# Kernel tuning notes

Hardware: AMD Instinct MI355X
Metric: run time of the kernel (lower is better)

## Reference

```python
import jax, jax.numpy as jnp
import numpy as np

EPS = 1e-6
CHUNK = 128  # chunk size for the chunked causal recurrence


def elu_feature_map(x):
    # fast_transformers default feature map: elu(x) + 1
    return jax.nn.elu(x) + 1.0


def causal_dot_product(Q, K, V):
    """out[l] = Q[l] @ sum_{l' <= l} K[l']^T V[l'].
    Q, K: (N, L, H, E); V: (N, L, H, D) -> (N, L, H, D).
    Chunked parallel recurrence: intra-chunk masked attention + inter-chunk state.
    """
    N, L, H, E = Q.shape
    D = V.shape[-1]
    C = CHUNK
    nc = L // C

    def to_chunks(x):
        # (N, L, H, F) -> (nc, N, H, C, F)
        F = x.shape[-1]
        return x.reshape(N, nc, C, H, F).transpose(1, 0, 3, 2, 4)

    Qc, Kc, Vc = to_chunks(Q), to_chunks(K), to_chunks(V)
    tri = jnp.tril(jnp.ones((C, C), dtype=Q.dtype))  # causal mask within chunk

    def step(state, qkv):  # state: (N, H, E, D)
        q, k, v = qkv  # (N,H,C,E), (N,H,C,E), (N,H,C,D)
        inter = jnp.einsum('nhce,nhed->nhcd', q, state)
        scores = jnp.einsum('nhce,nhfe->nhcf', q, k) * tri
        intra = jnp.einsum('nhcf,nhfd->nhcd', scores, v)
        state = state + jnp.einsum('nhce,nhcd->nhed', k, v)
        return state, inter + intra

    state0 = jnp.zeros((N, H, E, D), dtype=Q.dtype)
    _, out = jax.lax.scan(step, state0, (Qc, Kc, Vc))
    # (nc, N, H, C, D) -> (N, L, H, D)
    return out.transpose(1, 0, 3, 2, 4).reshape(N, L, H, D)


def setup_inputs() -> dict:
    key = jax.random.key(0)
    k1, k2, k3 = jax.random.split(key, 3)
    N, L, H, E = 4, 8192, 16, 64
    return {
        'queries': jax.random.normal(k1, (N, L, H, E), jnp.float32),
        'keys': jax.random.normal(k2, (N, L, H, E), jnp.float32),
        'values': jax.random.normal(k3, (N, L, H, E), jnp.float32),
        'key_mask': jnp.ones((N, L), dtype=bool),
    }


def reference(queries, keys, values, key_mask):
    # key_mask is accepted but unused, matching the original forward().
    Q = elu_feature_map(queries)
    K = elu_feature_map(keys)
    Z = 1.0 / (jnp.einsum('nlhi,nlhi->nlh', Q, jnp.cumsum(K, axis=1)) + EPS)
    V = causal_dot_product(Q, K, values)
    return V * Z[..., None]
```

## Files before the change

### kernel.cpp

```cpp
#include <hip/hip_runtime.h>
#include <hip/hip_bf16.h>


#define Nn   4
#define Ll   8192
#define Hh   16
#define NHh  64
#define CCH  64
#define LDB  72
#define SLOT 4160
#define EPSF 1e-6f

typedef __attribute__((ext_vector_type(8))) short short8;
typedef __attribute__((ext_vector_type(4))) float floatx4;

__device__ __forceinline__ float elu1(float x) {
  return x > 0.f ? x + 1.f : __expf(x);
}

__device__ __forceinline__ float4 elu4(float4 v) {
  v.x = elu1(v.x); v.y = elu1(v.y); v.z = elu1(v.z); v.w = elu1(v.w);
  return v;
}

__device__ __forceinline__ floatx4 mfma16(short8 a, short8 b, floatx4 c) {
  return __builtin_amdgcn_mfma_f32_16x16x32_bf16(a, b, c, 0, 0, 0);
}

__device__ __forceinline__ void bar_lgkm() {
  __builtin_amdgcn_s_waitcnt(0xc07f);
  __builtin_amdgcn_s_barrier();
  __builtin_amdgcn_sched_barrier(0);
}

__device__ __forceinline__ short8 frag_ld(const __hip_bfloat16* base, int row,
                                          int kh, int quad) {
  return *(const short8*)(base + row * LDB + kh * 32 + quad * 8);
}

__device__ __forceinline__ void st4bf(__hip_bfloat16* dst, float a, float b,
                                      float c, float d) {
  union { __hip_bfloat16 h[4]; uint2 u; } pk;
  pk.h[0] = __float2bfloat16(a); pk.h[1] = __float2bfloat16(b);
  pk.h[2] = __float2bfloat16(c); pk.h[3] = __float2bfloat16(d);
  *(uint2*)dst = pk.u;
}

__device__ __forceinline__ float bf2f(short s) {
  union { unsigned u; float f; } cv;
  cv.u = ((unsigned)(unsigned short)s) << 16;
  return cv.f;
}

__device__ __forceinline__ float sum8bf(short8 v) {
  float s = 0.f;
#pragma unroll
  for (int i = 0; i < 8; ++i) s += bf2f(v[i]);
  return s;
}

__global__ __launch_bounds__(256, 4) void la_pass1(
    const float* __restrict__ Kg, const float* __restrict__ Vg,
    float* __restrict__ ws, int G, int Lseg) {
  const int bid = blockIdx.x;
  const int nh = bid / G, g = bid % G;
  const int n = nh / Hh, h = nh % Hh;
  const int t = threadIdx.x;
  const int wave = t >> 6, lane = t & 63, m = lane & 15, quad = lane >> 4;
  const int jr0 = m * 4;
  const int er0 = wave * 16 + quad * 4;

  __shared__ __hip_bfloat16 Kt[2][64 * LDB];
  __shared__ __hip_bfloat16 Vt[2][64 * LDB];

  floatx4 Sacc[4];
  const floatx4 z4 = {0.f, 0.f, 0.f, 0.f};
#pragma unroll
  for (int b = 0; b < 4; ++b) Sacc[b] = z4;
  float kpriv[4] = {0.f, 0.f, 0.f, 0.f};

  const int nchunk = Lseg / CCH;

#define P1_LOAD(KR, VR, c_) do { \
    const size_t gb_ = \
        ((size_t)((n * Ll + g * Lseg + (c_) * CCH + jr0) * Hh + h)) * 64 + er0; \
    KR[0] = *(const float4*)(Kg + gb_);        \
    KR[1] = *(const float4*)(Kg + gb_ + 1024); \
    KR[2] = *(const float4*)(Kg + gb_ + 2048); \
    KR[3] = *(const float4*)(Kg + gb_ + 3072); \
    VR[0] = *(const float4*)(Vg + gb_);        \
    VR[1] = *(const float4*)(Vg + gb_ + 1024); \
    VR[2] = *(const float4*)(Vg + gb_ + 2048); \
    VR[3] = *(const float4*)(Vg + gb_ + 3072); \
  } while (0)

#define P1_STAGE(KR, VR, p_) do { \
    float4 e0 = elu4(KR[0]), e1 = elu4(KR[1]), e2 = elu4(KR[2]), e3 = elu4(KR[3]); \
    kpriv[0] += e0.x + e1.x + e2.x + e3.x; \
    kpriv[1] += e0.y + e1.y + e2.y + e3.y; \
    kpriv[2] += e0.z + e1.z + e2.z + e3.z; \
    kpriv[3] += e0.w + e1.w + e2.w + e3.w; \
    __hip_bfloat16* kt_ = Kt[p_]; __hip_bfloat16* vt_ = Vt[p_]; \
    st4bf(&kt_[(er0 + 0) * LDB + jr0], e0.x, e1.x, e2.x, e3.x); \
    st4bf(&kt_[(er0 + 1) * LDB + jr0], e0.y, e1.y, e2.y, e3.y); \
    st4bf(&kt_[(er0 + 2) * LDB + jr0], e0.z, e1.z, e2.z, e3.z); \
    st4bf(&kt_[(er0 + 3) * LDB + jr0], e0.w, e1.w, e2.w, e3.w); \
    st4bf(&vt_[(er0 + 0) * LDB + jr0], VR[0].x, VR[1].x, VR[2].x, VR[3].x); \
    st4bf(&vt_[(er0 + 1) * LDB + jr0], VR[0].y, VR[1].y, VR[2].y, VR[3].y); \
    st4bf(&vt_[(er0 + 2) * LDB + jr0], VR[0].z, VR[1].z, VR[2].z, VR[3].z); \
    st4bf(&vt_[(er0 + 3) * LDB + jr0], VR[0].w, VR[1].w, VR[2].w, VR[3].w); \
  } while (0)

#define P1_MFMA(p_) do { \
    const short8 a0 = frag_ld(Vt[p_], 16 * wave + m, 0, quad); \
    const short8 a1 = frag_ld(Vt[p_], 16 * wave + m, 1, quad); \
    __builtin_amdgcn_s_setprio(1); \
    _Pragma("unroll") \
    for (int b = 0; b < 4; ++b) { \
      Sacc[b] = mfma16(a0, frag_ld(Kt[p_], 16 * b + m, 0, quad), Sacc[b]); \
      Sacc[b] = mfma16(a1, frag_ld(Kt[p_], 16 * b + m, 1, quad), Sacc[b]); \
    } \
    __builtin_amdgcn_s_setprio(0); \
  } while (0)

  float4 ka[4], va[4], kb[4], vb[4];
  P1_LOAD(ka, va, 0);
  P1_LOAD(kb, vb, 1);
  P1_STAGE(ka, va, 0);
  for (int c = 0; c < nchunk; c += 2) {
    if (c + 2 < nchunk) P1_LOAD(ka, va, c + 2);
    bar_lgkm();
    P1_MFMA(0);
    P1_STAGE(kb, vb, 1);
    if (c + 3 < nchunk) P1_LOAD(kb, vb, c + 3);
    bar_lgkm();
    P1_MFMA(1);
    if (c + 2 < nchunk) P1_STAGE(ka, va, 0);
  }
#undef P1_LOAD
#undef P1_STAGE
#undef P1_MFMA

#pragma unroll
  for (int i = 0; i < 4; ++i) {
    kpriv[i] += __shfl_xor(kpriv[i], 1);
    kpriv[i] += __shfl_xor(kpriv[i], 2);
    kpriv[i] += __shfl_xor(kpriv[i], 4);
    kpriv[i] += __shfl_xor(kpriv[i], 8);
  }
  const size_t slot = (size_t)bid * SLOT;
#pragma unroll
  for (int b = 0; b < 4; ++b)
#pragma unroll
    for (int r = 0; r < 4; ++r) {
      const int d = 16 * wave + quad * 4 + r, e = 16 * b + m;
      ws[slot + d * 64 + e] = Sacc[b][r];
    }
  if (m == 0)
#pragma unroll
    for (int i = 0; i < 4; ++i) ws[slot + 4096 + er0 + i] = kpriv[i];
}

__global__ __launch_bounds__(256) void la_pass2(float* __restrict__ ws, int G) {
  const int nh = blockIdx.x / 17, part = blockIdx.x % 17;
  const int idx = part * 256 + threadIdx.x;
  if (idx >= SLOT) return;
  float run = 0.f;
  for (int g = 0; g < G; ++g) {
    const size_t base = (size_t)(nh * G + g) * SLOT;
    const float cur = ws[base + idx];
    ws[base + idx] = run;
    run += cur;
  }
}

__global__ __launch_bounds__(256, 4) void la_pass3(
    const float* __restrict__ Qg, const float* __restrict__ Kg,
    const float* __restrict__ Vg, const float* __restrict__ ws,
    float* __restrict__ out, int G, int Lseg, int has_prefix) {
  const int bid = blockIdx.x;
  const int nh = bid / G, g = bid % G;
  const int n = nh / Hh, h = nh % Hh;
  const int t = threadIdx.x;
  const int wave = t >> 6, lane = t & 63, m = lane & 15, quad = lane >> 4;
  const int row = t >> 2, q4 = t & 3;
  const int jr0 = m * 4;
  const int er0 = wave * 16 + quad * 4;

  __shared__ __hip_bfloat16 QPb[64 * LDB];
  __shared__ __hip_bfloat16 Kb [64 * LDB];
  __shared__ __hip_bfloat16 Ktb[64 * LDB];
  __shared__ __hip_bfloat16 Vtb[64 * LDB];
  __shared__ float ksum[64];
  __shared__ float kpart[4][64];

  const size_t slot = (size_t)bid * SLOT;
  floatx4 Sacc[4];
  const floatx4 z4 = {0.f, 0.f, 0.f, 0.f};
#pragma unroll
  for (int b = 0; b < 4; ++b) {
    Sacc[b] = z4;
    if (has_prefix) {
#pragma unroll
      for (int r = 0; r < 4; ++r)
        Sacc[b][r] = ws[slot + (16 * wave + quad * 4 + r) * 64 + 16 * b + m];
    }
  }
  if (t < 64) ksum[t] = has_prefix ? ws[slot + 4096 + t] : 0.f;

  const int nchunk = Lseg / CCH;
  for (int c = 0; c < nchunk; ++c) {
    const int lbase = g * Lseg + c * CCH;
    const size_t gbr = ((size_t)((n * Ll + lbase + row) * Hh + h)) * 64;
    const size_t gbv = ((size_t)((n * Ll + lbase + jr0) * Hh + h)) * 64 + er0;
    float4 qr[4], kr[4];
#pragma unroll
    for (int u = 0; u < 4; ++u) {
      const int col = u * 16 + q4 * 4;
      qr[u] = *(const float4*)(Qg + gbr + col);
      kr[u] = *(const float4*)(Kg + gbr + col);
    }
    float4 vr0 = *(const float4*)(Vg + gbv);
    float4 vr1 = *(const float4*)(Vg + gbv + 1024);
    float4 vr2 = *(const float4*)(Vg + gbv + 2048);
    float4 vr3 = *(const float4*)(Vg + gbv + 3072);
#pragma unroll
    for (int u = 0; u < 4; ++u) {
      const int col = u * 16 + q4 * 4;
      float4 qv = elu4(qr[u]);
      float4 kv = elu4(kr[u]);
      st4bf(&QPb[row * LDB + col], qv.x, qv.y, qv.z, qv.w);
      st4bf(&Kb [row * LDB + col], kv.x, kv.y, kv.z, kv.w);
      Ktb[(col + 0) * LDB + row] = __float2bfloat16(kv.x);
      Ktb[(col + 1) * LDB + row] = __float2bfloat16(kv.y);
      Ktb[(col + 2) * LDB + row] = __float2bfloat16(kv.z);
      Ktb[(col + 3) * LDB + row] = __float2bfloat16(kv.w);
    }
    bar_lgkm();

    const short8 qa0 = frag_ld(QPb, 16 * wave + m, 0, quad);
    const short8 qa1 = frag_ld(QPb, 16 * wave + m, 1, quad);
    floatx4 sc[4];
    __builtin_amdgcn_s_setprio(1);
#pragma unroll
    for (int b = 0; b < 4; ++b) {
      sc[b] = mfma16(qa0, frag_ld(Kb, 16 * b + m, 0, quad), z4);
      sc[b] = mfma16(qa1, frag_ld(Kb, 16 * b + m, 1, quad), sc[b]);
    }
    __builtin_amdgcn_s_setprio(0);
    float dpart = 0.f;
    {
      const float* ks0 = &ksum[quad * 8];
      const float* ks1 = &ksum[32 + quad * 8];
#pragma unroll
      for (int u = 0; u < 8; ++u) dpart += bf2f(qa0[u]) * ks0[u];
#pragma unroll
      for (int u = 0; u < 8; ++u) dpart += bf2f(qa1[u]) * ks1[u];
    }
    dpart += __shfl_xor(dpart, 16);
    dpart += __shfl_xor(dpart, 32);
    float z[4];
#pragma unroll
    for (int r = 0; r < 4; ++r) {
      const int i = 16 * wave + quad * 4 + r;
      float rs = 0.f;
#pragma unroll
      for (int b = 0; b < 4; ++b) {
        const int j = 16 * b + m;
        rs += (j <= i) ? sc[b][r] : 0.f;
      }
      rs += __shfl_xor(rs, 1);
      rs += __shfl_xor(rs, 2);
      rs += __shfl_xor(rs, 4);
      rs += __shfl_xor(rs, 8);
      const float den = __shfl(dpart, quad * 4 + r);
      z[r] = 1.f / (den + rs + EPSF);
    }
    bar_lgkm();

#pragma unroll
    for (int b = 0; b < 4; ++b)
#pragma unroll
      for (int r = 0; r < 4; ++r) {
        const int i = 16 * wave + quad * 4 + r, j = 16 * b + m;
        QPb[i * LDB + j] = __float2bfloat16(j <= i ? sc[b][r] : 0.f);
        Kb[i * LDB + j] = __float2bfloat16(Sacc[b][r]);
      }
    st4bf(&Vtb[(er0 + 0) * LDB + jr0], vr0.x, vr1.x, vr2.x, vr3.x);
    st4bf(&Vtb[(er0 + 1) * LDB + jr0], vr0.y, vr1.y, vr2.y, vr3.y);
    st4bf(&Vtb[(er0 + 2) * LDB + jr0], vr0.z, vr1.z, vr2.z, vr3.z);
    st4bf(&Vtb[(er0 + 3) * LDB + jr0], vr0.w, vr1.w, vr2.w, vr3.w);
    bar_lgkm();

    const short8 pa0 = frag_ld(QPb, 16 * wave + m, 0, quad);
    const short8 pa1 = frag_ld(QPb, 16 * wave + m, 1, quad);
    const short8 va0 = frag_ld(Vtb, 16 * wave + m, 0, quad);
    const short8 va1 = frag_ld(Vtb, 16 * wave + m, 1, quad);
    floatx4 O[4];
    __builtin_amdgcn_s_setprio(1);
#pragma unroll
    for (int b = 0; b < 4; ++b) {
      O[b] = mfma16(qa0, frag_ld(Kb, 16 * b + m, 0, quad), z4);
      O[b] = mfma16(qa1, frag_ld(Kb, 16 * b + m, 1, quad), O[b]);
      O[b] = mfma16(pa0, frag_ld(Vtb, 16 * b + m, 0, quad), O[b]);
      O[b] = mfma16(pa1, frag_ld(Vtb, 16 * b + m, 1, quad), O[b]);
      Sacc[b] = mfma16(va0, frag_ld(Ktb, 16 * b + m, 0, quad), Sacc[b]);
      Sacc[b] = mfma16(va1, frag_ld(Ktb, 16 * b + m, 1, quad), Sacc[b]);
    }
    __builtin_amdgcn_s_setprio(0);
    {
      const short8 x0 = *(const short8*)(&Ktb[lane * LDB + wave * 16]);
      const short8 x1 = *(const short8*)(&Ktb[lane * LDB + wave * 16 + 8]);
      kpart[wave][lane] = sum8bf(x0) + sum8bf(x1);
    }
    const size_t ob = ((size_t)((n * Ll + lbase) * Hh + h)) * 64;
#pragma unroll
    for (int r = 0; r < 4; ++r) {
      const int i = 16 * wave + quad * 4 + r;
#pragma unroll
      for (int b = 0; b < 4; ++b)
        out[ob + (size_t)i * (Hh * 64) + 16 * b + m] = O[b][r] * z[r];
    }
    bar_lgkm();
    if (t < 64)
      ksum[t] += kpart[0][t] + kpart[1][t] + kpart[2][t] + kpart[3][t];
  }
}

extern "C" void kernel_launch(void* const* d_in, const int* in_sizes, int n_in,
                              void* d_out, int out_size, void* d_ws, size_t ws_size,
                              hipStream_t stream) {
  (void)in_sizes; (void)n_in; (void)out_size;
  const float* Qg = (const float*)d_in[0];
  const float* Kg = (const float*)d_in[1];
  const float* Vg = (const float*)d_in[2];
  float* out = (float*)d_out;
  float* ws = (float*)d_ws;

  const size_t per_seg = (size_t)NHh * SLOT * sizeof(float);
  int G = 1;
  if (ws_size >= 16 * per_seg) G = 16;
  else if (ws_size >= 8 * per_seg) G = 8;
  else if (ws_size >= 4 * per_seg) G = 4;
  else if (ws_size >= 2 * per_seg) G = 2;
  const int Lseg = Ll / G;

  if (G > 1) {
    la_pass1<<<NHh * G, 256, 0, stream>>>(Kg, Vg, ws, G, Lseg);
    la_pass2<<<NHh * 17, 256, 0, stream>>>(ws, G);
  }
  la_pass3<<<NHh * G, 256, 0, stream>>>(Qg, Kg, Vg, ws, out, G, Lseg, G > 1 ? 1 : 0);
}
```

Measured before the change: 481.5 us.

## Fuse three passes into one kernel with atomic-flag cross-block prefix handoff

Merges the per-segment state pass, the prefix-scan pass and the output pass into a single kernel. Each block except the last computes its segment's KV state and key sum, publishes them with a release atomic bitmask, then waits on the masks of its predecessors and sums their states itself before running the output loop. This removes two kernel launches and the separate scan pass. In exchange, the last segment's work is serialized behind its predecessors, each block redundantly sums up to G-1 prefix slots, and correctness relies on every block in the grid being co-resident, otherwise the spin-wait can hang until its iteration cap.

```diff
diff --git a/kernel.cpp b/kernel.cpp
--- a/kernel.cpp
+++ b/kernel.cpp
@@ -59,29 +59,53 @@
   return s;
 }
 
-__global__ __launch_bounds__(256, 4) void la_pass1(
-    const float* __restrict__ Kg, const float* __restrict__ Vg,
-    float* __restrict__ ws, int G, int Lseg) {
+__device__ __forceinline__ float ld_agent_f32(const float* p) {
+  union { unsigned u; float f; } cv;
+  cv.u = __hip_atomic_load((const unsigned*)p, __ATOMIC_RELAXED,
+                           __HIP_MEMORY_SCOPE_AGENT);
+  return cv.f;
+}
+
+__global__ void la_zero(unsigned* __restrict__ masks) {
+  masks[threadIdx.x] = 0u;
+}
+
+__global__ __launch_bounds__(256, 4) void la_fused(
+    const float* __restrict__ Qg, const float* __restrict__ Kg,
+    const float* __restrict__ Vg, float* __restrict__ ws,
+    float* __restrict__ out, int G, int Lseg) {
   const int bid = blockIdx.x;
   const int nh = bid / G, g = bid % G;
   const int n = nh / Hh, h = nh % Hh;
   const int t = threadIdx.x;
   const int wave = t >> 6, lane = t & 63, m = lane & 15, quad = lane >> 4;
+  const int row = t >> 2, q4 = t & 3;
   const int jr0 = m * 4;
   const int er0 = wave * 16 + quad * 4;
 
-  __shared__ __hip_bfloat16 Kt[2][64 * LDB];
-  __shared__ __hip_bfloat16 Vt[2][64 * LDB];
+  __shared__ __hip_bfloat16 QPb[64 * LDB];
+  __shared__ __hip_bfloat16 Kb [64 * LDB];
+  __shared__ __hip_bfloat16 Ktb[64 * LDB];
+  __shared__ __hip_bfloat16 Vtb[64 * LDB];
+  __shared__ float ksum[64];
+  __shared__ float kpart[4][64];
+
+  unsigned* maskp =
+      (unsigned*)(ws + (size_t)NHh * G * SLOT) + nh;
 
   floatx4 Sacc[4];
   const floatx4 z4 = {0.f, 0.f, 0.f, 0.f};
 #pragma unroll
   for (int b = 0; b < 4; ++b) Sacc[b] = z4;
-  float kpriv[4] = {0.f, 0.f, 0.f, 0.f};
 
   const int nchunk = Lseg / CCH;
 
-#define P1_LOAD(KR, VR, c_) do { \
+  if (G > 1 && g < G - 1) {
+    __hip_bfloat16* kt0 = Ktb; __hip_bfloat16* vt0 = Vtb;
+    __hip_bfloat16* kt1 = QPb; __hip_bfloat16* vt1 = Kb;
+    float kpriv[4] = {0.f, 0.f, 0.f, 0.f};
+
+#define P_LOAD(KR, VR, c_) do { \
     const size_t gb_ = \
         ((size_t)((n * Ll + g * Lseg + (c_) * CCH + jr0) * Hh + h)) * 64 + er0; \
     KR[0] = *(const float4*)(Kg + gb_);        \
@@ -94,121 +118,107 @@
     VR[3] = *(const float4*)(Vg + gb_ + 3072); \
   } while (0)
 
-#define P1_STAGE(KR, VR, p_) do { \
+#define P_STAGE(KR, VR, kt_, vt_) do { \
     float4 e0 = elu4(KR[0]), e1 = elu4(KR[1]), e2 = elu4(KR[2]), e3 = elu4(KR[3]); \
     kpriv[0] += e0.x + e1.x + e2.x + e3.x; \
     kpriv[1] += e0.y + e1.y + e2.y + e3.y; \
     kpriv[2] += e0.z + e1.z + e2.z + e3.z; \
     kpriv[3] += e0.w + e1.w + e2.w + e3.w; \
-    __hip_bfloat16* kt_ = Kt[p_]; __hip_bfloat16* vt_ = Vt[p_]; \
-    st4bf(&kt_[(er0 + 0) * LDB + jr0], e0.x, e1.x, e2.x, e3.x); \
-    st4bf(&kt_[(er0 + 1) * LDB + jr0], e0.y, e1.y, e2.y, e3.y); \
-    st4bf(&kt_[(er0 + 2) * LDB + jr0], e0.z, e1.z, e2.z, e3.z); \
-    st4bf(&kt_[(er0 + 3) * LDB + jr0], e0.w, e1.w, e2.w, e3.w); \
-    st4bf(&vt_[(er0 + 0) * LDB + jr0], VR[0].x, VR[1].x, VR[2].x, VR[3].x); \
-    st4bf(&vt_[(er0 + 1) * LDB + jr0], VR[0].y, VR[1].y, VR[2].y, VR[3].y); \
-    st4bf(&vt_[(er0 + 2) * LDB + jr0], VR[0].z, VR[1].z, VR[2].z, VR[3].z); \
-    st4bf(&vt_[(er0 + 3) * LDB + jr0], VR[0].w, VR[1].w, VR[2].w, VR[3].w); \
+    st4bf(&(kt_)[(er0 + 0) * LDB + jr0], e0.x, e1.x, e2.x, e3.x); \
+    st4bf(&(kt_)[(er0 + 1) * LDB + jr0], e0.y, e1.y, e2.y, e3.y); \
+    st4bf(&(kt_)[(er0 + 2) * LDB + jr0], e0.z, e1.z, e2.z, e3.z); \
+    st4bf(&(kt_)[(er0 + 3) * LDB + jr0], e0.w, e1.w, e2.w, e3.w); \
+    st4bf(&(vt_)[(er0 + 0) * LDB + jr0], VR[0].x, VR[1].x, VR[2].x, VR[3].x); \
+    st4bf(&(vt_)[(er0 + 1) * LDB + jr0], VR[0].y, VR[1].y, VR[2].y, VR[3].y); \
+    st4bf(&(vt_)[(er0 + 2) * LDB + jr0], VR[0].z, VR[1].z, VR[2].z, VR[3].z); \
+    st4bf(&(vt_)[(er0 + 3) * LDB + jr0], VR[0].w, VR[1].w, VR[2].w, VR[3].w); \
   } while (0)
 
-#define P1_MFMA(p_) do { \
-    const short8 a0 = frag_ld(Vt[p_], 16 * wave + m, 0, quad); \
-    const short8 a1 = frag_ld(Vt[p_], 16 * wave + m, 1, quad); \
+#define P_MFMA(kt_, vt_) do { \
+    const short8 a0 = frag_ld((vt_), 16 * wave + m, 0, quad); \
+    const short8 a1 = frag_ld((vt_), 16 * wave + m, 1, quad); \
     __builtin_amdgcn_s_setprio(1); \
     _Pragma("unroll") \
     for (int b = 0; b < 4; ++b) { \
-      Sacc[b] = mfma16(a0, frag_ld(Kt[p_], 16 * b + m, 0, quad), Sacc[b]); \
-      Sacc[b] = mfma16(a1, frag_ld(Kt[p_], 16 * b + m, 1, quad), Sacc[b]); \
+      Sacc[b] = mfma16(a0, frag_ld((kt_), 16 * b + m, 0, quad), Sacc[b]); \
+      Sacc[b] = mfma16(a1, frag_ld((kt_), 16 * b + m, 1, quad), Sacc[b]); \
     } \
     __builtin_amdgcn_s_setprio(0); \
   } while (0)
 
-  float4 ka[4], va[4], kb[4], vb[4];
-  P1_LOAD(ka, va, 0);
-  P1_LOAD(kb, vb, 1);
-  P1_STAGE(ka, va, 0);
-  for (int c = 0; c < nchunk; c += 2) {
-    if (c + 2 < nchunk) P1_LOAD(ka, va, c + 2);
-    bar_lgkm();
-    P1_MFMA(0);
-    P1_STAGE(kb, vb, 1);
-    if (c + 3 < nchunk) P1_LOAD(kb, vb, c + 3);
-    bar_lgkm();
-    P1_MFMA(1);
-    if (c + 2 < nchunk) P1_STAGE(ka, va, 0);
+    float4 ka[4], va[4], kb2[4], vb2[4];
+    P_LOAD(ka, va, 0);
+    P_LOAD(kb2, vb2, 1);
+    P_STAGE(ka, va, kt0, vt0);
+    for (int c = 0; c < nchunk; c += 2) {
+      if (c + 2 < nchunk) P_LOAD(ka, va, c + 2);
+      bar_lgkm();
+      P_MFMA(kt0, vt0);
+      P_STAGE(kb2, vb2, kt1, vt1);
+      if (c + 3 < nchunk) P_LOAD(kb2, vb2, c + 3);
+      bar_lgkm();
+      P_MFMA(kt1, vt1);
+      if (c + 2 < nchunk) P_STAGE(ka, va, kt0, vt0);
+    }
+#undef P_LOAD
+#undef P_STAGE
+#undef P_MFMA
+
+#pragma unroll
+    for (int i = 0; i < 4; ++i) {
+      kpriv[i] += __shfl_xor(kpriv[i], 1);
+      kpriv[i] += __shfl_xor(kpriv[i], 2);
+      kpriv[i] += __shfl_xor(kpriv[i], 4);
+      kpriv[i] += __shfl_xor(kpriv[i], 8);
+    }
+    float* slotw = ws + (size_t)(nh * G + g) * SLOT;
+#pragma unroll
+    for (int b = 0; b < 4; ++b)
+#pragma unroll
+      for (int r = 0; r < 4; ++r) {
+        const int d = 16 * wave + quad * 4 + r, e = 16 * b + m;
+        slotw[d * 64 + e] = Sacc[b][r];
+      }
+    if (m == 0)
+#pragma unroll
+      for (int i = 0; i < 4; ++i) slotw[4096 + er0 + i] = kpriv[i];
+    __syncthreads();
+    if (t == 0)
+      __hip_atomic_fetch_or(maskp, 1u << g, __ATOMIC_RELEASE,
+                            __HIP_MEMORY_SCOPE_AGENT);
+#pragma unroll
+    for (int b = 0; b < 4; ++b) Sacc[b] = z4;
   }
-#undef P1_LOAD
-#undef P1_STAGE
-#undef P1_MFMA
-
-#pragma unroll
-  for (int i = 0; i < 4; ++i) {
-    kpriv[i] += __shfl_xor(kpriv[i], 1);
-    kpriv[i] += __shfl_xor(kpriv[i], 2);
-    kpriv[i] += __shfl_xor(kpriv[i], 4);
-    kpriv[i] += __shfl_xor(kpriv[i], 8);
+
+  float ks_init = 0.f;
+  if (G > 1 && g > 0) {
+    const unsigned need = (1u << g) - 1u;
+    if (t == 0) {
+      int iter = 0;
+      while ((__hip_atomic_load(maskp, __ATOMIC_ACQUIRE,
+                                __HIP_MEMORY_SCOPE_AGENT) & need) != need &&
+             iter < (1 << 24)) {
+        __builtin_amdgcn_s_sleep(2);
+        ++iter;
+      }
+    }
+    __syncthreads();
+    (void)__hip_atomic_load(maskp, __ATOMIC_ACQUIRE, __HIP_MEMORY_SCOPE_AGENT);
+    for (int gp = 0; gp < g; ++gp) {
+      const float* base = ws + (size_t)(nh * G + gp) * SLOT;
+#pragma unroll
+      for (int b = 0; b < 4; ++b)
+#pragma unroll
+        for (int r = 0; r < 4; ++r) {
+          const int d = 16 * wave + quad * 4 + r, e = 16 * b + m;
+          Sacc[b][r] += ld_agent_f32(base + d * 64 + e);
+        }
+      if (t < 64) ks_init += ld_agent_f32(base + 4096 + t);
+    }
   }
-  const size_t slot = (size_t)bid * SLOT;
-#pragma unroll
-  for (int b = 0; b < 4; ++b)
-#pragma unroll
-    for (int r = 0; r < 4; ++r) {
-      const int d = 16 * wave + quad * 4 + r, e = 16 * b + m;
-      ws[slot + d * 64 + e] = Sacc[b][r];
-    }
-  if (m == 0)
-#pragma unroll
-    for (int i = 0; i < 4; ++i) ws[slot + 4096 + er0 + i] = kpriv[i];
-}
-
-__global__ __launch_bounds__(256) void la_pass2(float* __restrict__ ws, int G) {
-  const int nh = blockIdx.x / 17, part = blockIdx.x % 17;
-  const int idx = part * 256 + threadIdx.x;
-  if (idx >= SLOT) return;
-  float run = 0.f;
-  for (int g = 0; g < G; ++g) {
-    const size_t base = (size_t)(nh * G + g) * SLOT;
-    const float cur = ws[base + idx];
-    ws[base + idx] = run;
-    run += cur;
-  }
-}
-
-__global__ __launch_bounds__(256, 4) void la_pass3(
-    const float* __restrict__ Qg, const float* __restrict__ Kg,
-    const float* __restrict__ Vg, const float* __restrict__ ws,
-    float* __restrict__ out, int G, int Lseg, int has_prefix) {
-  const int bid = blockIdx.x;
-  const int nh = bid / G, g = bid % G;
-  const int n = nh / Hh, h = nh % Hh;
-  const int t = threadIdx.x;
-  const int wave = t >> 6, lane = t & 63, m = lane & 15, quad = lane >> 4;
-  const int row = t >> 2, q4 = t & 3;
-  const int jr0 = m * 4;
-  const int er0 = wave * 16 + quad * 4;
-
-  __shared__ __hip_bfloat16 QPb[64 * LDB];
-  __shared__ __hip_bfloat16 Kb [64 * LDB];
-  __shared__ __hip_bfloat16 Ktb[64 * LDB];
-  __shared__ __hip_bfloat16 Vtb[64 * LDB];
-  __shared__ float ksum[64];
-  __shared__ float kpart[4][64];
-
-  const size_t slot = (size_t)bid * SLOT;
-  floatx4 Sacc[4];
-  const floatx4 z4 = {0.f, 0.f, 0.f, 0.f};
-#pragma unroll
-  for (int b = 0; b < 4; ++b) {
-    Sacc[b] = z4;
-    if (has_prefix) {
-#pragma unroll
-      for (int r = 0; r < 4; ++r)
-        Sacc[b][r] = ws[slot + (16 * wave + quad * 4 + r) * 64 + 16 * b + m];
-    }
-  }
-  if (t < 64) ksum[t] = has_prefix ? ws[slot + 4096 + t] : 0.f;
-
-  const int nchunk = Lseg / CCH;
+  if (t < 64) ksum[t] = ks_init;
+  __syncthreads();
+
   for (int c = 0; c < nchunk; ++c) {
     const int lbase = g * Lseg + c * CCH;
     const size_t gbr = ((size_t)((n * Ll + lbase + row) * Hh + h)) * 64;
@@ -339,15 +349,15 @@
 
   const size_t per_seg = (size_t)NHh * SLOT * sizeof(float);
   int G = 1;
-  if (ws_size >= 16 * per_seg) G = 16;
-  else if (ws_size >= 8 * per_seg) G = 8;
-  else if (ws_size >= 4 * per_seg) G = 4;
-  else if (ws_size >= 2 * per_seg) G = 2;
+  if (ws_size >= 16 * per_seg + 1024) G = 16;
+  else if (ws_size >= 8 * per_seg + 1024) G = 8;
+  else if (ws_size >= 4 * per_seg + 1024) G = 4;
+  else if (ws_size >= 2 * per_seg + 1024) G = 2;
   const int Lseg = Ll / G;
 
   if (G > 1) {
-    la_pass1<<<NHh * G, 256, 0, stream>>>(Kg, Vg, ws, G, Lseg);
-    la_pass2<<<NHh * 17, 256, 0, stream>>>(ws, G);
+    unsigned* masks = (unsigned*)(ws + (size_t)NHh * G * SLOT);
+    la_zero<<<1, NHh, 0, stream>>>(masks);
   }
-  la_pass3<<<NHh * G, 256, 0, stream>>>(Qg, Kg, Vg, ws, out, G, Lseg, G > 1 ? 1 : 0);
-}
+  la_fused<<<NHh * G, 256, 0, stream>>>(Qg, Kg, Vg, ws, out, G, Lseg);
+}
```

After: 609.2 us. +26.5%, slower.

## Split pass1 sequence across waves with private LDS tiles and cross-wave reduction

Applied to the files above, without the earlier changes.

Pass 1 now gives each wave its own contiguous quarter of the segment, processed in 32-position chunks in private LDS tiles. This removes the block-wide barriers inside the loop. Each wave holds the full 64x64 state in 16 MFMA accumulators and fills it from its own K/V loads. The per-wave partial states and key sums are then reduced through shared memory at the end. The cost is more accumulator registers, a K dimension of 32 per chunk, and no software prefetch double-buffering, which may expose global load latency.

```diff
diff --git a/kernel.cpp b/kernel.cpp
--- a/kernel.cpp
+++ b/kernel.cpp
@@ -38,6 +38,14 @@
   return *(const short8*)(base + row * LDB + kh * 32 + quad * 8);
 }
 
+__device__ __forceinline__ short8 frag36(const short* base, int row, int quad) {
+  union { short8 v; uint2 p[2]; } u;
+  const short* p = base + row * 36 + quad * 8;
+  u.p[0] = *(const uint2*)(p);
+  u.p[1] = *(const uint2*)(p + 4);
+  return u.v;
+}
+
 __device__ __forceinline__ void st4bf(__hip_bfloat16* dst, float a, float b,
                                       float c, float d) {
   union { __hip_bfloat16 h[4]; uint2 u; } pk;
@@ -67,98 +75,116 @@
   const int n = nh / Hh, h = nh % Hh;
   const int t = threadIdx.x;
   const int wave = t >> 6, lane = t & 63, m = lane & 15, quad = lane >> 4;
-  const int jr0 = m * 4;
-  const int er0 = wave * 16 + quad * 4;
-
-  __shared__ __hip_bfloat16 Kt[2][64 * LDB];
-  __shared__ __hip_bfloat16 Vt[2][64 * LDB];
-
-  floatx4 Sacc[4];
+  const int pg = lane & 7, cg = lane >> 3;
+  const int j0 = pg * 4, c0 = cg * 8;
+
+  __shared__ __align__(16) short smem[18432];
+  short* Kt = smem + wave * 2304;
+  short* Vt = smem + 9216 + wave * 2304;
+
+  floatx4 acc[4][4];
   const floatx4 z4 = {0.f, 0.f, 0.f, 0.f};
 #pragma unroll
-  for (int b = 0; b < 4; ++b) Sacc[b] = z4;
-  float kpriv[4] = {0.f, 0.f, 0.f, 0.f};
-
-  const int nchunk = Lseg / CCH;
-
-#define P1_LOAD(KR, VR, c_) do { \
-    const size_t gb_ = \
-        ((size_t)((n * Ll + g * Lseg + (c_) * CCH + jr0) * Hh + h)) * 64 + er0; \
-    KR[0] = *(const float4*)(Kg + gb_);        \
-    KR[1] = *(const float4*)(Kg + gb_ + 1024); \
-    KR[2] = *(const float4*)(Kg + gb_ + 2048); \
-    KR[3] = *(const float4*)(Kg + gb_ + 3072); \
-    VR[0] = *(const float4*)(Vg + gb_);        \
-    VR[1] = *(const float4*)(Vg + gb_ + 1024); \
-    VR[2] = *(const float4*)(Vg + gb_ + 2048); \
-    VR[3] = *(const float4*)(Vg + gb_ + 3072); \
-  } while (0)
-
-#define P1_STAGE(KR, VR, p_) do { \
-    float4 e0 = elu4(KR[0]), e1 = elu4(KR[1]), e2 = elu4(KR[2]), e3 = elu4(KR[3]); \
-    kpriv[0] += e0.x + e1.x + e2.x + e3.x; \
-    kpriv[1] += e0.y + e1.y + e2.y + e3.y; \
-    kpriv[2] += e0.z + e1.z + e2.z + e3.z; \
-    kpriv[3] += e0.w + e1.w + e2.w + e3.w; \
-    __hip_bfloat16* kt_ = Kt[p_]; __hip_bfloat16* vt_ = Vt[p_]; \
-    st4bf(&kt_[(er0 + 0) * LDB + jr0], e0.x, e1.x, e2.x, e3.x); \
-    st4bf(&kt_[(er0 + 1) * LDB + jr0], e0.y, e1.y, e2.y, e3.y); \
-    st4bf(&kt_[(er0 + 2) * LDB + jr0], e0.z, e1.z, e2.z, e3.z); \
-    st4bf(&kt_[(er0 + 3) * LDB + jr0], e0.w, e1.w, e2.w, e3.w); \
-    st4bf(&vt_[(er0 + 0) * LDB + jr0], VR[0].x, VR[1].x, VR[2].x, VR[3].x); \
-    st4bf(&vt_[(er0 + 1) * LDB + jr0], VR[0].y, VR[1].y, VR[2].y, VR[3].y); \
-    st4bf(&vt_[(er0 + 2) * LDB + jr0], VR[0].z, VR[1].z, VR[2].z, VR[3].z); \
-    st4bf(&vt_[(er0 + 3) * LDB + jr0], VR[0].w, VR[1].w, VR[2].w, VR[3].w); \
-  } while (0)
-
-#define P1_MFMA(p_) do { \
-    const short8 a0 = frag_ld(Vt[p_], 16 * wave + m, 0, quad); \
-    const short8 a1 = frag_ld(Vt[p_], 16 * wave + m, 1, quad); \
-    __builtin_amdgcn_s_setprio(1); \
-    _Pragma("unroll") \
-    for (int b = 0; b < 4; ++b) { \
-      Sacc[b] = mfma16(a0, frag_ld(Kt[p_], 16 * b + m, 0, quad), Sacc[b]); \
-      Sacc[b] = mfma16(a1, frag_ld(Kt[p_], 16 * b + m, 1, quad), Sacc[b]); \
-    } \
-    __builtin_amdgcn_s_setprio(0); \
-  } while (0)
-
-  float4 ka[4], va[4], kb[4], vb[4];
-  P1_LOAD(ka, va, 0);
-  P1_LOAD(kb, vb, 1);
-  P1_STAGE(ka, va, 0);
-  for (int c = 0; c < nchunk; c += 2) {
-    if (c + 2 < nchunk) P1_LOAD(ka, va, c + 2);
-    bar_lgkm();
-    P1_MFMA(0);
-    P1_STAGE(kb, vb, 1);
-    if (c + 3 < nchunk) P1_LOAD(kb, vb, c + 3);
-    bar_lgkm();
-    P1_MFMA(1);
-    if (c + 2 < nchunk) P1_STAGE(ka, va, 0);
-  }
-#undef P1_LOAD
-#undef P1_STAGE
-#undef P1_MFMA
-
-#pragma unroll
-  for (int i = 0; i < 4; ++i) {
-    kpriv[i] += __shfl_xor(kpriv[i], 1);
-    kpriv[i] += __shfl_xor(kpriv[i], 2);
-    kpriv[i] += __shfl_xor(kpriv[i], 4);
-    kpriv[i] += __shfl_xor(kpriv[i], 8);
-  }
+  for (int a = 0; a < 4; ++a)
+#pragma unroll
+    for (int b = 0; b < 4; ++b) acc[a][b] = z4;
+  float kpriv[8] = {0.f, 0.f, 0.f, 0.f, 0.f, 0.f, 0.f, 0.f};
+
+  const int nwc = Lseg >> 7;
+  const int base_pos = g * Lseg + wave * (Lseg >> 2);
+
+  for (int ch = 0; ch < nwc; ++ch) {
+    const int pos = base_pos + ch * 32 + j0;
+    const size_t gb = ((size_t)((n * Ll + pos) * Hh + h)) * 64 + c0;
+    float4 ka0 = *(const float4*)(Kg + gb);
+    float4 ka1 = *(const float4*)(Kg + gb + 1024);
+    float4 ka2 = *(const float4*)(Kg + gb + 2048);
+    float4 ka3 = *(const float4*)(Kg + gb + 3072);
+    float4 kb0 = *(const float4*)(Kg + gb + 4);
+    float4 kb1 = *(const float4*)(Kg + gb + 1028);
+    float4 kb2 = *(const float4*)(Kg + gb + 2052);
+    float4 kb3 = *(const float4*)(Kg + gb + 3076);
+    ka0 = elu4(ka0); ka1 = elu4(ka1); ka2 = elu4(ka2); ka3 = elu4(ka3);
+    kb0 = elu4(kb0); kb1 = elu4(kb1); kb2 = elu4(kb2); kb3 = elu4(kb3);
+    kpriv[0] += ka0.x + ka1.x + ka2.x + ka3.x;
+    kpriv[1] += ka0.y + ka1.y + ka2.y + ka3.y;
+    kpriv[2] += ka0.z + ka1.z + ka2.z + ka3.z;
+    kpriv[3] += ka0.w + ka1.w + ka2.w + ka3.w;
+    kpriv[4] += kb0.x + kb1.x + kb2.x + kb3.x;
+    kpriv[5] += kb0.y + kb1.y + kb2.y + kb3.y;
+    kpriv[6] += kb0.z + kb1.z + kb2.z + kb3.z;
+    kpriv[7] += kb0.w + kb1.w + kb2.w + kb3.w;
+    __hip_bfloat16* ktb = (__hip_bfloat16*)Kt;
+    st4bf(&ktb[(c0 + 0) * 36 + j0], ka0.x, ka1.x, ka2.x, ka3.x);
+    st4bf(&ktb[(c0 + 1) * 36 + j0], ka0.y, ka1.y, ka2.y, ka3.y);
+    st4bf(&ktb[(c0 + 2) * 36 + j0], ka0.z, ka1.z, ka2.z, ka3.z);
+    st4bf(&ktb[(c0 + 3) * 36 + j0], ka0.w, ka1.w, ka2.w, ka3.w);
+    st4bf(&ktb[(c0 + 4) * 36 + j0], kb0.x, kb1.x, kb2.x, kb3.x);
+    st4bf(&ktb[(c0 + 5) * 36 + j0], kb0.y, kb1.y, kb2.y, kb3.y);
+    st4bf(&ktb[(c0 + 6) * 36 + j0], kb0.z, kb1.z, kb2.z, kb3.z);
+    st4bf(&ktb[(c0 + 7) * 36 + j0], kb0.w, kb1.w, kb2.w, kb3.w);
+    float4 va0 = *(const float4*)(Vg + gb);
+    float4 va1 = *(const float4*)(Vg + gb + 1024);
+    float4 va2 = *(const float4*)(Vg + gb + 2048);
+    float4 va3 = *(const float4*)(Vg + gb + 3072);
+    float4 vb0 = *(const float4*)(Vg + gb + 4);
+    float4 vb1 = *(const float4*)(Vg + gb + 1028);
+    float4 vb2 = *(const float4*)(Vg + gb + 2052);
+    float4 vb3 = *(const float4*)(Vg + gb + 3076);
+    __hip_bfloat16* vtb = (__hip_bfloat16*)Vt;
+    st4bf(&vtb[(c0 + 0) * 36 + j0], va0.x, va1.x, va2.x, va3.x);
+    st4bf(&vtb[(c0 + 1) * 36 + j0], va0.y, va1.y, va2.y, va3.y);
+    st4bf(&vtb[(c0 + 2) * 36 + j0], va0.z, va1.z, va2.z, va3.z);
+    st4bf(&vtb[(c0 + 3) * 36 + j0], va0.w, va1.w, va2.w, va3.w);
+    st4bf(&vtb[(c0 + 4) * 36 + j0], vb0.x, vb1.x, vb2.x, vb3.x);
+    st4bf(&vtb[(c0 + 5) * 36 + j0], vb0.y, vb1.y, vb2.y, vb3.y);
+    st4bf(&vtb[(c0 + 6) * 36 + j0], vb0.z, vb1.z, vb2.z, vb3.z);
+    st4bf(&vtb[(c0 + 7) * 36 + j0], vb0.w, vb1.w, vb2.w, vb3.w);
+    short8 af[4], bf[4];
+#pragma unroll
+    for (int db = 0; db < 4; ++db) af[db] = frag36(Vt, 16 * db + m, quad);
+#pragma unroll
+    for (int eb = 0; eb < 4; ++eb) bf[eb] = frag36(Kt, 16 * eb + m, quad);
+    __builtin_amdgcn_s_setprio(1);
+#pragma unroll
+    for (int db = 0; db < 4; ++db)
+#pragma unroll
+      for (int eb = 0; eb < 4; ++eb)
+        acc[db][eb] = mfma16(af[db], bf[eb], acc[db][eb]);
+    __builtin_amdgcn_s_setprio(0);
+  }
+
+  __syncthreads();
+  float* redf = (float*)smem;
   const size_t slot = (size_t)bid * SLOT;
 #pragma unroll
-  for (int b = 0; b < 4; ++b)
-#pragma unroll
-    for (int r = 0; r < 4; ++r) {
-      const int d = 16 * wave + quad * 4 + r, e = 16 * b + m;
-      ws[slot + d * 64 + e] = Sacc[b][r];
-    }
-  if (m == 0)
-#pragma unroll
-    for (int i = 0; i < 4; ++i) ws[slot + 4096 + er0 + i] = kpriv[i];
+  for (int db = 0; db < 4; ++db) {
+#pragma unroll
+    for (int eb = 0; eb < 4; ++eb)
+#pragma unroll
+      for (int r = 0; r < 4; ++r)
+        redf[wave * 1024 + (quad * 4 + r) * 64 + 16 * eb + m] = acc[db][eb][r];
+    __syncthreads();
+#pragma unroll
+    for (int u = 0; u < 4; ++u) {
+      const int i = t + 256 * u;
+      const float s = redf[i] + redf[1024 + i] + redf[2048 + i] + redf[3072 + i];
+      ws[slot + (16 * db + (i >> 6)) * 64 + (i & 63)] = s;
+    }
+    __syncthreads();
+  }
+#pragma unroll
+  for (int u = 0; u < 8; ++u) {
+    kpriv[u] += __shfl_xor(kpriv[u], 1);
+    kpriv[u] += __shfl_xor(kpriv[u], 2);
+    kpriv[u] += __shfl_xor(kpriv[u], 4);
+  }
+  if (pg == 0)
+#pragma unroll
+    for (int u = 0; u < 8; ++u) redf[wave * 64 + c0 + u] = kpriv[u];
+  __syncthreads();
+  if (t < 64)
+    ws[slot + 4096 + t] = redf[t] + redf[64 + t] + redf[128 + t] + redf[192 + t];
 }
 
 __global__ __launch_bounds__(256) void la_pass2(float* __restrict__ ws, int G) {
```

Result: no change. 475.1 us (-1.3%).
